# Optimization experiments

Hardware: AMD Instinct MI355X
Metric: run time of the kernel (lower is better)

Reference implementation:

```python
import jax, jax.numpy as jnp
import numpy as np

BS, TLEN, NNODE, DIM = 32, 6, 4, 1500
HID = 128; D2 = 2 * HID
LSTMH, LSTMO, KCONV = 64, 128, 3
CONV_OUT = 191
DECAY = 0.7
WIN, STRIDES = (2, 2), (1, 2)
FEAT_IN = LSTMO * CONV_OUT  # 24448


def _bn(x, p, axis):
    # eval-mode BatchNorm: p = [gamma, beta, running_mean, running_var] stacked [4, C]
    sh = [1] * x.ndim; sh[axis] = -1
    g, b, m, v = (p[i].reshape(sh) for i in range(4))
    return (x - m) * (g * jax.lax.rsqrt(v + 1e-5)) + b


def _conv1d(x, w, pad):  # x [B,C,L], w [O,I,K]
    return jax.lax.conv_general_dilated(x, w, (1,), [(pad, pad)],
                                        dimension_numbers=('NCH', 'OIH', 'NCH'))


def _maxpool2(x):  # MaxPool1d(kernel=2, stride=2, padding=1) with -inf padding
    x = jnp.pad(x, ((0, 0), (0, 0), (1, 1)), constant_values=-jnp.inf)
    return jax.lax.reduce_window(x, -jnp.inf, jax.lax.max, (1, 1, 2), (1, 1, 2), 'VALID')


def _mpnn_block(x, w, s, gw, gb, bnA, tw, tb, bnM):
    # x: [bs, tlen, ns, d]; Conv_GraphST windowing + dot-graph + masked adj + 1-hop MPNN + mean pool
    bs, tlen, ns, d = x.shape
    nw = (tlen - w) // s + 1
    con = jnp.stack([x[:, j * s:j * s + w] for j in range(nw)], axis=1)  # [bs,nw,w,ns,d]
    Xc = con.reshape(bs * nw, w * ns, d)  # node index = t*ns + sensor (time-major)
    f = Xc @ gw + gb
    N = w * ns
    eye = jnp.eye(N, dtype=x.dtype)
    Adj = jnp.einsum('bnd,bmd->bnm', f, f)
    Adj = jax.nn.softmax(jax.nn.leaky_relu(Adj - eye * 1e8), axis=-1) + eye
    t = jnp.arange(N) // ns
    mask = DECAY ** jnp.abs(t[:, None] - t[None, :]).astype(x.dtype)  # Mask_Matrix decay
    Adj = Adj * mask
    Xb = _bn(Xc, bnA, -1)  # BN over feature channel (transpose-BN-transpose in torch)
    h = jnp.einsum('bnm,bmd->bnd', Adj, Xb) @ tw + tb
    h = jax.nn.leaky_relu(_bn(h, bnM, -1))
    return h.reshape(bs, nw, w, ns, -1).mean(axis=2)  # mean pool over window-time


def _pos_encoding(tlen, d):
    pos = jnp.arange(tlen, dtype=jnp.float32)[:, None]
    div = jnp.exp(jnp.arange(0, d, 2, dtype=jnp.float32) * (-np.log(100.0) / d))
    pe = jnp.zeros((tlen, d), jnp.float32)
    return pe.at[:, 0::2].set(jnp.sin(pos * div)).at[:, 1::2].set(jnp.cos(pos * div))


def reference(X, conv1_w, bn1, conv2_w, bn2, conv3_w, bn3,
              map2_w, map2_b, bn_map2,
              g1_w, g1_b, bnA1, th1_w, th1_b, bnM1,
              g2_w, g2_b, bnA2, th2_w, th2_b, bnM2,
              fc1_w, fc1_b, fc2_w, fc2_b, fc3_w, fc3_b, fc4_w, fc4_b):
    X = X.reshape(BS, TLEN, NNODE, -1)
    B = BS * TLEN * NNODE
    a = jnp.transpose(X.reshape(B, -1, 1), (0, 2, 1))  # [B,1,L]
    a = _maxpool2(jax.nn.relu(_bn(_conv1d(a, conv1_w, KCONV // 2), bn1, 1)))
    a = _maxpool2(jax.nn.relu(_bn(_conv1d(a, conv2_w, 2), bn2, 1)))
    a = _maxpool2(jax.nn.relu(_bn(_conv1d(a, conv3_w, 3), bn3, 1)))  # [B,LSTMO,CONV_OUT]
    a = a.reshape(B, -1)
    a = _bn(a @ map2_w + map2_b, bn_map2, -1)
    a = a.reshape(BS, TLEN, NNODE, D2)
    a = a + _pos_encoding(TLEN, D2)[None, :, None, :]  # PE over time, per (batch, node)
    out1 = _mpnn_block(a, WIN[0], STRIDES[0], g1_w, g1_b, bnA1, th1_w, th1_b, bnM1)  # [32,5,4,128]
    out2 = _mpnn_block(a, WIN[1], STRIDES[1], g2_w, g2_b, bnA2, th2_w, th2_b, bnM2)  # [32,3,4,128]
    feats = jnp.concatenate([out1.reshape(BS, -1), out2.reshape(BS, -1)], axis=-1)  # [32,4096]
    h = jax.nn.relu(feats @ fc1_w + fc1_b)
    h = jax.nn.relu(h @ fc2_w + fc2_b)
    h = jax.nn.relu(h @ fc3_w + fc3_b)
    return h @ fc4_w + fc4_b


def setup_inputs():
    key = jax.random.key(0)
    ks = iter(jax.random.split(key, 80))
    def rn(shape, scale=1.0):
        return scale * jax.random.normal(next(ks), shape, jnp.float32)
    def bn(c):
        return jnp.stack([1.0 + 0.1 * rn((c,)), 0.1 * rn((c,)), 0.1 * rn((c,)),
                          1.0 + 0.5 * jax.random.uniform(next(ks), (c,), jnp.float32)])
    def lin(i, o):
        return rn((i, o), 1.0 / np.sqrt(i))
    return {
        'X': rn((BS, TLEN, NNODE, DIM)),
        'conv1_w': rn((LSTMH, 1, KCONV), 0.3),
        'bn1': bn(LSTMH),
        'conv2_w': rn((2 * LSTMH, LSTMH, KCONV), 1.0 / np.sqrt(LSTMH * KCONV)),
        'bn2': bn(2 * LSTMH),
        'conv3_w': rn((LSTMO, 2 * LSTMH, KCONV), 1.0 / np.sqrt(2 * LSTMH * KCONV)),
        'bn3': bn(LSTMO),
        'map2_w': lin(FEAT_IN, D2), 'map2_b': rn((D2,), 0.01), 'bn_map2': bn(D2),
        'g1_w': lin(D2, D2), 'g1_b': rn((D2,), 0.01), 'bnA1': bn(D2),
        'th1_w': lin(D2, HID), 'th1_b': rn((HID,), 0.01), 'bnM1': bn(HID),
        'g2_w': lin(D2, D2), 'g2_b': rn((D2,), 0.01), 'bnA2': bn(D2),
        'th2_w': lin(D2, HID), 'th2_b': rn((HID,), 0.01), 'bnM2': bn(HID),
        'fc1_w': lin(4096, D2), 'fc1_b': rn((D2,), 0.01),
        'fc2_w': lin(D2, D2), 'fc2_b': rn((D2,), 0.01),
        'fc3_w': lin(D2, HID), 'fc3_b': rn((HID,), 0.01),
        'fc4_w': lin(HID, 5), 'fc4_b': rn((5,), 0.01),
    }
```

## Files before the change

kernel.cpp:

```cpp
#include <hip/hip_runtime.h>
#include <hip/hip_bf16.h>

#define L1X   1500
#define L1P   751
#define C1    64
#define L2P   377
#define C2    128
#define L3P   191
#define C3    128
#define FEATK 24448
#define D2    256
#define HIDN  128

#define SK      32
#define KCHUNK  764
#define NIT     191

typedef __attribute__((ext_vector_type(8))) short bf16x8;
typedef __attribute__((ext_vector_type(4))) float f32x4;

__device__ __forceinline__ short f2bf(float x) {
    union { float f; unsigned u; } v; v.f = x;
    unsigned r = (v.u + 0x7FFFu + ((v.u >> 16) & 1u)) >> 16;
    return (short)r;
}
__device__ __forceinline__ float bf2f(short s) {
    union { float f; unsigned u; } v; v.u = ((unsigned)(unsigned short)s) << 16;
    return v.f;
}

template<int IC, int KB>
__global__ __launch_bounds__(256)
void k_wprep(const float* __restrict__ w, short* __restrict__ WtHi,
             short* __restrict__ WtLo)
{
    int idx = blockIdx.x * 256 + threadIdx.x;
    if (idx >= 3 * KB * 4 * 128 * 8) return;
    int i    = idx & 7;
    int rest = idx >> 3;
    int c    = rest & 127; rest >>= 7;
    int sub  = rest & 3;   rest >>= 2;
    int kb   = rest % KB;
    int tap  = rest / KB;
    int ic   = kb * 32 + sub * 8 + i;
    float x  = w[(c * IC + ic) * 3 + tap];
    short h  = f2bf(x);
    WtHi[idx] = h;
    WtLo[idx] = f2bf(x - bf2f(h));
}

template<int IC, int KB, int CONVLEN, int POOLLEN>
__device__ __forceinline__
void conv_mfma_core(const short* __restrict__ WtHi, const short* __restrict__ WtLo,
                    const short* lhi, const short* llo,
                    const float* sc, const float* bc,
                    float* __restrict__ outp, int P0)
{
    const int lane = threadIdx.x & 63;
    const int wave = threadIdx.x >> 6;
    const int l15  = lane & 15;
    const int sub  = lane >> 4;

    f32x4 acc[2][8];
    #pragma unroll
    for (int mf = 0; mf < 2; ++mf)
        #pragma unroll
        for (int nf = 0; nf < 8; ++nf)
            acc[mf][nf] = (f32x4){0.f, 0.f, 0.f, 0.f};

    #pragma unroll
    for (int tap = 0; tap < 3; ++tap) {
        #pragma unroll
        for (int kb = 0; kb < KB; ++kb) {
            bf16x8 ah[2], al[2];
            #pragma unroll
            for (int mf = 0; mf < 2; ++mf) {
                int r = wave * 32 + mf * 16 + l15 + tap;
                int chunk = (kb * 4 + sub) ^ (r & 7);
                int off = r * IC + chunk * 8;
                ah[mf] = *(const bf16x8*)(lhi + off);
                al[mf] = *(const bf16x8*)(llo + off);
            }
            const short* wbh = WtHi + (size_t)(((tap * KB + kb) * 4 + sub) * 128) * 8;
            const short* wbl = WtLo + (size_t)(((tap * KB + kb) * 4 + sub) * 128) * 8;
            #pragma unroll
            for (int nf = 0; nf < 8; ++nf) {
                bf16x8 bh = *(const bf16x8*)(wbh + (nf * 16 + l15) * 8);
                bf16x8 bl = *(const bf16x8*)(wbl + (nf * 16 + l15) * 8);
                #pragma unroll
                for (int mf = 0; mf < 2; ++mf) {
                    acc[mf][nf] = __builtin_amdgcn_mfma_f32_16x16x32_bf16(ah[mf], bh, acc[mf][nf], 0, 0, 0);
                    acc[mf][nf] = __builtin_amdgcn_mfma_f32_16x16x32_bf16(ah[mf], bl, acc[mf][nf], 0, 0, 0);
                    acc[mf][nf] = __builtin_amdgcn_mfma_f32_16x16x32_bf16(al[mf], bh, acc[mf][nf], 0, 0, 0);
                }
            }
        }
    }

    #pragma unroll
    for (int mf = 0; mf < 2; ++mf) {
        int mbase = wave * 32 + mf * 16 + sub * 4;
        #pragma unroll
        for (int nf = 0; nf < 8; ++nf) {
            int c = nf * 16 + l15;
            float s = sc[c], bb = bc[c];
            float v[4];
            #pragma unroll
            for (int rg = 0; rg < 4; ++rg) {
                int p = P0 + mbase + rg;
                float x = fmaxf(acc[mf][nf][rg] * s + bb, 0.f);
                v[rg] = (p >= 0 && p < CONVLEN) ? x : 0.f;
            }
            int i0 = (P0 + mbase + 1) >> 1;
            float u0 = fmaxf(v[0], v[1]);
            float u1 = fmaxf(v[2], v[3]);
            if (i0 < POOLLEN)     outp[(size_t)i0 * 128 + c] = u0;
            if (i0 + 1 < POOLLEN) outp[(size_t)(i0 + 1) * 128 + c] = u1;
        }
    }
}

__global__ __launch_bounds__(256)
void k_conv2_mfma(const float* __restrict__ X, const float* __restrict__ w1,
                  const float* __restrict__ bn1,
                  const short* __restrict__ Wt2hi, const short* __restrict__ Wt2lo,
                  const float* __restrict__ bn2, float* __restrict__ pool2t,
                  int b_off)
{
    const int blk = blockIdx.x;
    const int bl  = blk / 6, t = blk % 6;
    const int b   = b_off + bl;
    const int P0  = 128 * t - 1;
    const int T0  = 128 * t - 3;
    const int X0  = 256 * t - 8;

    __shared__ __align__(16) float xw[264];
    __shared__ __align__(16) short t1h[130 * 64];
    __shared__ __align__(16) short t1l[130 * 64];
    __shared__ float sb1s[64], sb1b[64], sc2[128], bc2[128];

    const int tid = threadIdx.x;
    for (int g = tid; g < 262; g += 256) {
        int xi = X0 + g;
        xw[g] = (xi >= 0 && xi < L1X) ? X[(size_t)b * L1X + xi] : 0.f;
    }
    if (tid < 64) {
        float s = bn1[tid] * rsqrtf(bn1[192 + tid] + 1e-5f);
        sb1s[tid] = s;
        sb1b[tid] = bn1[64 + tid] - bn1[128 + tid] * s;
    }
    if (tid < 128) {
        float s = bn2[tid] * rsqrtf(bn2[384 + tid] + 1e-5f);
        sc2[tid] = s;
        bc2[tid] = bn2[128 + tid] - bn2[256 + tid] * s;
    }
    __syncthreads();

    for (int idx = tid; idx < 130 * 64; idx += 256) {
        int r = idx >> 6, c = idx & 63;
        int tt = T0 + r;
        float val = 0.f;
        if (tt >= 0 && tt <= 750) {
            float wk0 = w1[c * 3], wk1 = w1[c * 3 + 1], wk2 = w1[c * 3 + 2];
            float s = sb1s[c], bias = sb1b[c];
            float v0 = 0.f, v1 = 0.f;
            int li = 2 * r;
            if (tt >= 1)
                v0 = fmaxf((wk0 * xw[li] + wk1 * xw[li + 1] + wk2 * xw[li + 2]) * s + bias, 0.f);
            if (tt <= 749)
                v1 = fmaxf((wk0 * xw[li + 1] + wk1 * xw[li + 2] + wk2 * xw[li + 3]) * s + bias, 0.f);
            val = fmaxf(v0, v1);
        }
        short h = f2bf(val);
        int chunk = (c >> 3) ^ (r & 7);
        int off = r * 64 + chunk * 8 + (c & 7);
        t1h[off] = h;
        t1l[off] = f2bf(val - bf2f(h));
    }
    __syncthreads();

    conv_mfma_core<64, 2, 753, 377>(Wt2hi, Wt2lo, t1h, t1l, sc2, bc2,
                                    pool2t + (size_t)bl * L2P * 128, P0);
}

__global__ __launch_bounds__(256)
void k_conv3_mfma(const float* __restrict__ pool2t,
                  const short* __restrict__ Wt3hi, const short* __restrict__ Wt3lo,
                  const float* __restrict__ bn3, float* __restrict__ pool3t,
                  int b_off)
{
    const int blk = blockIdx.x;
    const int bl  = blk / 3, t = blk % 3;
    const int b   = b_off + bl;
    const int P0  = 128 * t - 1;
    const int I0  = 128 * t - 4;

    __shared__ __align__(16) short t2h[130 * 128];
    __shared__ __align__(16) short t2l[130 * 128];
    __shared__ float sc3[128], bc3[128];

    const int tid = threadIdx.x;
    if (tid < 128) {
        float s = bn3[tid] * rsqrtf(bn3[384 + tid] + 1e-5f);
        sc3[tid] = s;
        bc3[tid] = bn3[128 + tid] - bn3[256 + tid] * s;
    }

    const float* src = pool2t + (size_t)bl * L2P * 128;
    for (int idx = tid; idx < 130 * 32; idx += 256) {
        int r = idx >> 5, q = idx & 31;
        int pr = I0 + r;
        float4 v = make_float4(0.f, 0.f, 0.f, 0.f);
        if (pr >= 0 && pr < L2P) v = *(const float4*)(src + (size_t)pr * 128 + q * 4);
        int chunk = (q >> 1) ^ (r & 7);
        int off = r * 128 + chunk * 8 + (q & 1) * 4;
        *(short4*)(t2h + off) = make_short4(f2bf(v.x), f2bf(v.y), f2bf(v.z), f2bf(v.w));
        short l0 = f2bf(v.x - bf2f(f2bf(v.x)));
        short l1 = f2bf(v.y - bf2f(f2bf(v.y)));
        short l2 = f2bf(v.z - bf2f(f2bf(v.z)));
        short l3 = f2bf(v.w - bf2f(f2bf(v.w)));
        *(short4*)(t2l + off) = make_short4(l0, l1, l2, l3);
    }
    __syncthreads();

    conv_mfma_core<128, 4, 381, 191>(Wt3hi, Wt3lo, t2h, t2l, sc3, bc3,
                                     pool3t + (size_t)b * L3P * 128, P0);
}

__global__ __launch_bounds__(256)
void k_map2_gemm(const float* __restrict__ A, const float* __restrict__ W,
                 float* __restrict__ part)
{
    const int bid = blockIdx.x;
    const int kt  = bid / 24;
    const int rem = bid % 24;
    const int mt  = rem >> 1;
    const int nt  = rem & 1;

    __shared__ __align__(16) float At[2][4][64];
    __shared__ __align__(16) float Bt[2][4][128];

    const int tid = threadIdx.x;
    const int m0  = (tid & 15) * 4;
    const int n0  = (tid >> 4) * 8;

    const int arow = tid >> 2;
    const int akk  = tid & 3;
    const int bk   = tid >> 6;
    const int bc   = (tid & 63) * 2;

    const float* Aptr = A + (size_t)(mt * 64 + arow) * FEATK + kt * KCHUNK + akk;

    #define BROW(it) (W + (size_t)((((kt*KCHUNK + (it)*4 + bk) & 127) * 191 + \
                                    ((kt*KCHUNK + (it)*4 + bk) >> 7))) * D2 + nt*128 + bc)

    float acc[4][8];
    #pragma unroll
    for (int i = 0; i < 4; ++i)
        #pragma unroll
        for (int j = 0; j < 8; ++j) acc[i][j] = 0.f;

    float  a_reg = Aptr[0];
    float2 b_reg = *(const float2*)(BROW(0));
    At[0][akk][arow] = a_reg;
    *(float2*)&Bt[0][bk][bc] = b_reg;

    int cur = 0;
    for (int it = 0; it < NIT; ++it) {
        __syncthreads();
        if (it + 1 < NIT) {
            a_reg = Aptr[(it + 1) * 4];
            b_reg = *(const float2*)(BROW(it + 1));
        }
        #pragma unroll
        for (int k = 0; k < 4; ++k) {
            float4 a0 = *(const float4*)&At[cur][k][m0];
            float4 b0 = *(const float4*)&Bt[cur][k][n0];
            float4 b1 = *(const float4*)&Bt[cur][k][n0 + 4];
            float av[4] = {a0.x, a0.y, a0.z, a0.w};
            float bv[8] = {b0.x, b0.y, b0.z, b0.w, b1.x, b1.y, b1.z, b1.w};
            #pragma unroll
            for (int i = 0; i < 4; ++i)
                #pragma unroll
                for (int j = 0; j < 8; ++j)
                    acc[i][j] += av[i] * bv[j];
        }
        if (it + 1 < NIT) {
            At[cur ^ 1][akk][arow] = a_reg;
            *(float2*)&Bt[cur ^ 1][bk][bc] = b_reg;
        }
        cur ^= 1;
    }
    #undef BROW

    float* P = part + ((size_t)kt * 768) * D2;
    #pragma unroll
    for (int i = 0; i < 4; ++i) {
        int grow = mt * 64 + m0 + i;
        float* dst = P + (size_t)grow * D2 + nt * 128 + n0;
        *(float4*)(dst)     = make_float4(acc[i][0], acc[i][1], acc[i][2], acc[i][3]);
        *(float4*)(dst + 4) = make_float4(acc[i][4], acc[i][5], acc[i][6], acc[i][7]);
    }
}

__global__ __launch_bounds__(256)
void k_map2fin(const float* __restrict__ part, const float* __restrict__ mb,
               const float* __restrict__ bn, float* __restrict__ out)
{
    const int row = blockIdx.x;
    const int n   = threadIdx.x;
    float acc = 0.f;
    #pragma unroll
    for (int kt = 0; kt < SK; ++kt)
        acc += part[((size_t)kt * 768 + row) * D2 + n];

    float s    = bn[n] * rsqrtf(bn[768 + n] + 1e-5f);
    float beta = bn[256 + n];
    float mu   = bn[512 + n];
    float bias = mb[n];
    int   jj   = n >> 1;
    float freq = expf((float)(2 * jj) * (-4.605170185988092f / 256.f));
    int   t    = (row >> 2) % 6;
    float ang  = (float)t * freq;
    float pe   = (n & 1) ? cosf(ang) : sinf(ang);
    out[(size_t)row * D2 + n] = (acc + bias - mu) * s + beta + pe;
}

__global__ __launch_bounds__(256)
void k_mpnn(const float* __restrict__ a_pe, const float* __restrict__ gw,
            const float* __restrict__ gb, const float* __restrict__ bnA,
            const float* __restrict__ tw, const float* __restrict__ tb_,
            const float* __restrict__ bnM, float* __restrict__ feats,
            int nw, int stride, int base)
{
    const int g  = blockIdx.x;
    const int b  = g / nw, wi = g % nw;
    const int tid = threadIdx.x;

    __shared__ float Xc[8][256];
    __shared__ float Xb[8][256];
    __shared__ float Fs[8][256];
    __shared__ float Adj[8][8];
    __shared__ float hsm[8][128];

    for (int e = tid; e < 2048; e += 256) {
        int nn = e >> 8, d = e & 255;
        int tt = nn >> 2, sn = nn & 3;
        float v = a_pe[(((size_t)(b * 6) + (wi * stride + tt)) * 4 + sn) * D2 + d];
        Xc[nn][d] = v;
        float s = bnA[d] * rsqrtf(bnA[768 + d] + 1e-5f);
        Xb[nn][d] = (v - bnA[512 + d]) * s + bnA[256 + d];
    }
    __syncthreads();

    {
        const int d = tid;
        #pragma unroll
        for (int nn = 0; nn < 8; ++nn) {
            float acc = gb[d];
            for (int k = 0; k < 256; ++k) acc += Xc[nn][k] * gw[(size_t)k * D2 + d];
            Fs[nn][d] = acc;
        }
    }
    __syncthreads();

    if (tid < 64) {
        int nn = tid >> 3, m = tid & 7;
        float s = 0.f;
        for (int d = 0; d < 256; ++d) s += Fs[nn][d] * Fs[m][d];
        if (nn == m) s -= 1e8f;
        s = (s > 0.f) ? s : 0.01f * s;
        Adj[nn][m] = s;
    }
    __syncthreads();

    if (tid < 8) {
        int nn = tid;
        float mx = -1e30f;
        for (int m = 0; m < 8; ++m) mx = fmaxf(mx, Adj[nn][m]);
        float ex[8]; float sum = 0.f;
        for (int m = 0; m < 8; ++m) { ex[m] = expf(Adj[nn][m] - mx); sum += ex[m]; }
        float inv = 1.f / sum;
        for (int m = 0; m < 8; ++m) {
            float v = ex[m] * inv + ((nn == m) ? 1.f : 0.f);
            v *= ((nn >> 2) == (m >> 2)) ? 1.f : 0.7f;
            Adj[nn][m] = v;
        }
    }
    __syncthreads();

    {
        const int d = tid;
        float hm[8];
        #pragma unroll
        for (int nn = 0; nn < 8; ++nn) {
            float a = 0.f;
            #pragma unroll
            for (int m = 0; m < 8; ++m) a += Adj[nn][m] * Xb[m][d];
            hm[nn] = a;
        }
        #pragma unroll
        for (int nn = 0; nn < 8; ++nn) Fs[nn][d] = hm[nn];
    }
    __syncthreads();

    {
        const int o = tid & 127, half = tid >> 7;
        float ms  = bnM[o] * rsqrtf(bnM[384 + o] + 1e-5f);
        float mbe = bnM[128 + o], mmu = bnM[256 + o];
        #pragma unroll
        for (int q = 0; q < 4; ++q) {
            int nn = half + 2 * q;
            float acc = tb_[o];
            for (int d = 0; d < 256; ++d) acc += Fs[nn][d] * tw[(size_t)d * HIDN + o];
            float y = (acc - mmu) * ms + mbe;
            hsm[nn][o] = (y > 0.f) ? y : 0.01f * y;
        }
    }
    __syncthreads();

    for (int e = tid; e < 512; e += 256) {
        int sn = e >> 7, o = e & 127;
        feats[(size_t)b * 4096 + base + (wi * 4 + sn) * HIDN + o] =
            0.5f * (hsm[sn][o] + hsm[4 + sn][o]);
    }
}

__global__ __launch_bounds__(256)
void k_fc(const float* __restrict__ feats,
          const float* __restrict__ w1f, const float* __restrict__ b1f,
          const float* __restrict__ w2f, const float* __restrict__ b2f,
          const float* __restrict__ w3f, const float* __restrict__ b3f,
          const float* __restrict__ w4f, const float* __restrict__ b4f,
          float* __restrict__ out)
{
    const int b = blockIdx.x;
    __shared__ float row[4096];
    __shared__ float h1[256], h2[256], h3[128];
    for (int e = threadIdx.x; e < 4096; e += 256) row[e] = feats[(size_t)b * 4096 + e];
    __syncthreads();
    const int n = threadIdx.x;
    {
        float acc = b1f[n];
        for (int f = 0; f < 4096; ++f) acc += row[f] * w1f[(size_t)f * 256 + n];
        h1[n] = fmaxf(acc, 0.f);
    }
    __syncthreads();
    {
        float acc = b2f[n];
        for (int k = 0; k < 256; ++k) acc += h1[k] * w2f[(size_t)k * 256 + n];
        h2[n] = fmaxf(acc, 0.f);
    }
    __syncthreads();
    if (n < 128) {
        float acc = b3f[n];
        for (int k = 0; k < 256; ++k) acc += h2[k] * w3f[(size_t)k * 128 + n];
        h3[n] = fmaxf(acc, 0.f);
    }
    __syncthreads();
    if (n < 5) {
        float acc = b4f[n];
        for (int k = 0; k < 128; ++k) acc += h3[k] * w4f[(size_t)k * 5 + n];
        out[b * 5 + n] = acc;
    }
}

extern "C" void kernel_launch(void* const* d_in, const int* in_sizes, int n_in,
                              void* d_out, int out_size, void* d_ws, size_t ws_size,
                              hipStream_t stream)
{
    const float* X      = (const float*)d_in[0];
    const float* w1     = (const float*)d_in[1];
    const float* bn1    = (const float*)d_in[2];
    const float* w2     = (const float*)d_in[3];
    const float* bn2    = (const float*)d_in[4];
    const float* w3     = (const float*)d_in[5];
    const float* bn3    = (const float*)d_in[6];
    const float* map2w  = (const float*)d_in[7];
    const float* map2b  = (const float*)d_in[8];
    const float* bnm2   = (const float*)d_in[9];
    const float* g1w    = (const float*)d_in[10];
    const float* g1b    = (const float*)d_in[11];
    const float* bnA1   = (const float*)d_in[12];
    const float* th1w   = (const float*)d_in[13];
    const float* th1b   = (const float*)d_in[14];
    const float* bnM1   = (const float*)d_in[15];
    const float* g2w    = (const float*)d_in[16];
    const float* g2b    = (const float*)d_in[17];
    const float* bnA2   = (const float*)d_in[18];
    const float* th2w   = (const float*)d_in[19];
    const float* th2b   = (const float*)d_in[20];
    const float* bnM2   = (const float*)d_in[21];
    const float* fc1w   = (const float*)d_in[22];
    const float* fc1b   = (const float*)d_in[23];
    const float* fc2w   = (const float*)d_in[24];
    const float* fc2b   = (const float*)d_in[25];
    const float* fc3w   = (const float*)d_in[26];
    const float* fc3b   = (const float*)d_in[27];
    const float* fc4w   = (const float*)d_in[28];
    const float* fc4b   = (const float*)d_in[29];
    float* out = (float*)d_out;

    float* ws = (float*)d_ws;
    const size_t N_P2C = (size_t)192 * L2P * 128;
    const size_t N_P3  = (size_t)768 * L3P * 128;
    float* pool2t = ws;
    float* pool3t = ws + N_P2C;
    float* a_pe   = pool3t + N_P3;
    float* feats  = a_pe + (size_t)768 * D2;
    short* Wt2hi  = (short*)(feats + (size_t)32 * 4096);
    short* Wt2lo  = Wt2hi + 24576;
    short* Wt3hi  = Wt2lo + 24576;
    short* Wt3lo  = Wt3hi + 49152;
    float* part   = ws;

    k_wprep<64, 2><<<96, 256, 0, stream>>>(w2, Wt2hi, Wt2lo);
    k_wprep<128, 4><<<192, 256, 0, stream>>>(w3, Wt3hi, Wt3lo);

    for (int boff = 0; boff < 768; boff += 192) {
        k_conv2_mfma<<<192 * 6, 256, 0, stream>>>(X, w1, bn1, Wt2hi, Wt2lo, bn2,
                                                  pool2t, boff);
        k_conv3_mfma<<<192 * 3, 256, 0, stream>>>(pool2t, Wt3hi, Wt3lo, bn3,
                                                  pool3t, boff);
    }
    k_map2_gemm<<<768, 256, 0, stream>>>(pool3t, map2w, part);
    k_map2fin<<<768, 256, 0, stream>>>(part, map2b, bnm2, a_pe);
    k_mpnn<<<160, 256, 0, stream>>>(a_pe, g1w, g1b, bnA1, th1w, th1b, bnM1,
                                    feats, 5, 1, 0);
    k_mpnn<<<96, 256, 0, stream>>>(a_pe, g2w, g2b, bnA2, th2w, th2b, bnM2,
                                   feats, 3, 2, 2560);
    k_fc<<<32, 256, 0, stream>>>(feats, fc1w, fc1b, fc2w, fc2b, fc3w, fc3b,
                                 fc4w, fc4b, out);
}
```

Baseline: 790.6 us.

## Split FC1 into parallel split-K kernel and pad map2 shared tile

The first fully connected layer moves into its own kernel. That kernel uses 128 blocks, each covering a 256-wide K chunk and a 32-column slice for all 32 batch rows, so each weight is read once instead of once per batch row. Partial sums go to workspace and are reduced in the remaining FC kernel. Separately, the map2 GEMM's shared A tile is padded to reduce LDS bank conflicts. The cost is one extra launch and a partial-sum buffer in workspace.

```diff
diff --git a/kernel.cpp b/kernel.cpp
--- a/kernel.cpp
+++ b/kernel.cpp
@@ -237,7 +237,7 @@
     const int mt  = rem >> 1;
     const int nt  = rem & 1;
 
-    __shared__ __align__(16) float At[2][4][64];
+    __shared__ __align__(16) float At[2][4][68];
     __shared__ __align__(16) float Bt[2][4][128];
 
     const int tid = threadIdx.x;
@@ -427,22 +427,54 @@
 }
 
 __global__ __launch_bounds__(256)
-void k_fc(const float* __restrict__ feats,
-          const float* __restrict__ w1f, const float* __restrict__ b1f,
-          const float* __restrict__ w2f, const float* __restrict__ b2f,
-          const float* __restrict__ w3f, const float* __restrict__ b3f,
-          const float* __restrict__ w4f, const float* __restrict__ b4f,
-          float* __restrict__ out)
+void k_fc1(const float* __restrict__ feats, const float* __restrict__ w1f,
+           float* __restrict__ partfc)
+{
+    const int kc = blockIdx.x >> 3;
+    const int nc = blockIdx.x & 7;
+    const int tid = threadIdx.x;
+
+    __shared__ float fst[32 * 257];
+
+    for (int idx = tid; idx < 32 * 256; idx += 256) {
+        int r = idx >> 8, k = idx & 255;
+        fst[r * 257 + k] = feats[(size_t)r * 4096 + kc * 256 + k];
+    }
+    __syncthreads();
+
+    const int c  = tid & 31;
+    const int rg = tid >> 5;
+    const float* wp = w1f + (size_t)(kc * 256) * 256 + nc * 32 + c;
+
+    float acc[4] = {0.f, 0.f, 0.f, 0.f};
+    for (int k = 0; k < 256; ++k) {
+        float wv = wp[(size_t)k * 256];
+        #pragma unroll
+        for (int j = 0; j < 4; ++j)
+            acc[j] += fst[(rg * 4 + j) * 257 + k] * wv;
+    }
+    #pragma unroll
+    for (int j = 0; j < 4; ++j)
+        partfc[((size_t)kc * 32 + rg * 4 + j) * 256 + nc * 32 + c] = acc[j];
+}
+
+__global__ __launch_bounds__(256)
+void k_fc_rest(const float* __restrict__ partfc,
+               const float* __restrict__ b1f,
+               const float* __restrict__ w2f, const float* __restrict__ b2f,
+               const float* __restrict__ w3f, const float* __restrict__ b3f,
+               const float* __restrict__ w4f, const float* __restrict__ b4f,
+               float* __restrict__ out)
 {
     const int b = blockIdx.x;
-    __shared__ float row[4096];
+    const int n = threadIdx.x;
     __shared__ float h1[256], h2[256], h3[128];
-    for (int e = threadIdx.x; e < 4096; e += 256) row[e] = feats[(size_t)b * 4096 + e];
-    __syncthreads();
-    const int n = threadIdx.x;
+
     {
         float acc = b1f[n];
-        for (int f = 0; f < 4096; ++f) acc += row[f] * w1f[(size_t)f * 256 + n];
+        #pragma unroll
+        for (int kc = 0; kc < 16; ++kc)
+            acc += partfc[((size_t)kc * 32 + b) * 256 + n];
         h1[n] = fmaxf(acc, 0.f);
     }
     __syncthreads();
@@ -512,6 +544,7 @@
     short* Wt2lo  = Wt2hi + 24576;
     short* Wt3hi  = Wt2lo + 24576;
     short* Wt3lo  = Wt3hi + 49152;
+    float* partfc = (float*)(Wt3lo + 49152);
     float* part   = ws;
 
     k_wprep<64, 2><<<96, 256, 0, stream>>>(w2, Wt2hi, Wt2lo);
@@ -529,6 +562,7 @@
                                     feats, 5, 1, 0);
     k_mpnn<<<96, 256, 0, stream>>>(a_pe, g2w, g2b, bnA2, th2w, th2b, bnM2,
                                    feats, 3, 2, 2560);
-    k_fc<<<32, 256, 0, stream>>>(feats, fc1w, fc1b, fc2w, fc2b, fc3w, fc3b,
-                                 fc4w, fc4b, out);
-}
+    k_fc1<<<128, 256, 0, stream>>>(feats, fc1w, partfc);
+    k_fc_rest<<<32, 256, 0, stream>>>(partfc, fc1b, fc2w, fc2b, fc3w, fc3b,
+                                      fc4w, fc4b, out);
+}
```

Measured after the change: 717.9 us. -9.2%, faster.
